# Kernel optimization log

Hardware: AMD Instinct MI355X
Metric: run time of the kernel (lower is better)

Reference implementation:

```python
import jax, jax.numpy as jnp
import numpy as np
import math

B, T, D, H = 2, 2048, 1024, 16
HD = D // H
FF = 4 * D
EPS = 1e-5


def rmsnorm(x, w):
    norm = jax.lax.rsqrt(jnp.mean(x * x, axis=-1, keepdims=True) + EPS)
    return x * norm * w


def setup_inputs() -> dict:
    key = jax.random.key(0)
    ks = jax.random.split(key, 10)
    s = 0.02
    x = jax.random.normal(ks[0], (B, T, D), dtype=jnp.float32)
    causal_mask = jnp.tril(jnp.ones((1, T, T), dtype=jnp.int32))
    # weights stored (in, out) so y = x @ W (equivalent to torch Linear with W.T)
    Wq = jax.random.normal(ks[1], (D, D), dtype=jnp.float32) * s
    Wk = jax.random.normal(ks[2], (D, D), dtype=jnp.float32) * s
    Wv = jax.random.normal(ks[3], (D, D), dtype=jnp.float32) * s
    Wo = jax.random.normal(ks[4], (D, D), dtype=jnp.float32) * s
    bo = jnp.zeros((D,), dtype=jnp.float32)
    W1 = jax.random.normal(ks[5], (D, FF), dtype=jnp.float32) * s
    b1 = jnp.zeros((FF,), dtype=jnp.float32)
    W2 = jax.random.normal(ks[6], (FF, D), dtype=jnp.float32) * s
    b2 = jnp.zeros((D,), dtype=jnp.float32)
    g_attn = jnp.ones((D,), dtype=jnp.float32)
    g_ff = jnp.ones((D,), dtype=jnp.float32)
    return dict(x=x, causal_mask=causal_mask, Wq=Wq, Wk=Wk, Wv=Wv, Wo=Wo, bo=bo,
                W1=W1, b1=b1, W2=W2, b2=b2, g_attn=g_attn, g_ff=g_ff)


def reference(x, causal_mask, Wq, Wk, Wv, Wo, bo, W1, b1, W2, b2, g_attn, g_ff):
    b, t, d = x.shape
    xa = rmsnorm(x, g_attn)
    # project and split heads: (b, h, t, hd)
    q = (xa @ Wq).reshape(b, t, H, HD).transpose(0, 2, 1, 3)
    k = (xa @ Wk).reshape(b, t, H, HD).transpose(0, 2, 1, 3)
    v = (xa @ Wv).reshape(b, t, H, HD).transpose(0, 2, 1, 3)
    scores = jnp.einsum('bhqd,bhkd->bhqk', q, k) / math.sqrt(HD)
    mask = causal_mask[:, None, :t, :t]  # (1,1,t,t)
    scores = jnp.where(mask == 0, jnp.float32(-1e9), scores)
    probs = jax.nn.softmax(scores, axis=-1)
    attn = jnp.einsum('bhqk,bhkd->bhqd', probs, v)
    attn = attn.transpose(0, 2, 1, 3).reshape(b, t, d)
    x = x + attn @ Wo + bo
    xf = rmsnorm(x, g_ff)
    h = jax.nn.silu(xf @ W1 + b1)
    x = x + h @ W2 + b2
    return x
```

## Files before the change

### kernel.cpp

```cpp
#include <hip/hip_runtime.h>
#include <hip/hip_bf16.h>
#include <cstdint>
#include <cstddef>

#define Bn 2
#define Tn 2048
#define Dn 1024
#define Hn 16
#define HDn 64
#define FFn 4096
#define Mrows (Bn*Tn)

typedef __bf16 bf16x8 __attribute__((ext_vector_type(8)));
typedef float  f32x4  __attribute__((ext_vector_type(4)));

__device__ __forceinline__ unsigned short f2bf(float f) {
  unsigned int u = __float_as_uint(f);
  unsigned int r = (u + 0x7FFFu + ((u >> 16) & 1u)) >> 16;
  return (unsigned short)r;
}

__device__ __forceinline__ void gload_lds16(const unsigned short* g, unsigned short* l) {
  __builtin_amdgcn_global_load_lds(
      (const __attribute__((address_space(1))) unsigned int*)g,
      (__attribute__((address_space(3))) unsigned int*)l, 16, 0, 0);
}

__device__ __forceinline__ f32x4 mfma16(bf16x8 a, bf16x8 b, f32x4 c) {
  return __builtin_amdgcn_mfma_f32_16x16x32_bf16(a, b, c, 0, 0, 0);
}

__global__ void cast_transpose(const float* __restrict__ in, unsigned short* __restrict__ out,
                               int R, int C) {
  __shared__ float tile[32][33];
  int c0 = blockIdx.x * 32, r0 = blockIdx.y * 32;
  int x = threadIdx.x, y = threadIdx.y;
  #pragma unroll
  for (int i = 0; i < 32; i += 8)
    tile[y + i][x] = in[(size_t)(r0 + y + i) * C + c0 + x];
  __syncthreads();
  #pragma unroll
  for (int i = 0; i < 32; i += 8)
    out[(size_t)(c0 + y + i) * R + r0 + x] = f2bf(tile[x][y + i]);
}

__global__ __launch_bounds__(256) void rmsnorm_cast(const float* __restrict__ x,
                                                    const float* __restrict__ g,
                                                    unsigned short* __restrict__ out) {
  __shared__ float ssum[4];
  int row = blockIdx.x;
  int tid = threadIdx.x;
  const float4* xr = (const float4*)(x + (size_t)row * Dn);
  float4 v = xr[tid];
  float ss = v.x * v.x + v.y * v.y + v.z * v.z + v.w * v.w;
  #pragma unroll
  for (int m = 32; m; m >>= 1) ss += __shfl_xor(ss, m);
  if ((tid & 63) == 0) ssum[tid >> 6] = ss;
  __syncthreads();
  float tot = ssum[0] + ssum[1] + ssum[2] + ssum[3];
  float nrm = rsqrtf(tot * (1.0f / Dn) + 1e-5f);
  float4 gv = ((const float4*)g)[tid];
  ushort4 o;
  o.x = f2bf(v.x * nrm * gv.x);
  o.y = f2bf(v.y * nrm * gv.y);
  o.z = f2bf(v.z * nrm * gv.z);
  o.w = f2bf(v.w * nrm * gv.w);
  ((ushort4*)out)[(size_t)row * (Dn / 4) + tid] = o;
}

#define BM 128
#define BN 128
#define BK 64
template <int EPI>
__global__ __launch_bounds__(256, 2) void gemm_bt(
    const unsigned short* __restrict__ A, const unsigned short* __restrict__ Bt,
    unsigned short* __restrict__ outB, unsigned short* __restrict__ outB2,
    unsigned short* __restrict__ outB3, float* __restrict__ outF,
    const float* __restrict__ bias, const float* __restrict__ resid,
    int Mdim, int Ndim, int Kdim) {
  __shared__ __align__(16) unsigned short As[BM * BK];
  __shared__ __align__(16) unsigned short Bs[BN * BK];
  const int tid = threadIdx.x;
  const int lane = tid & 63, w = tid >> 6;
  const int wr = w >> 1, wc = w & 1;
  const int lr = lane & 15, lg = lane >> 4;
  const int m0 = blockIdx.y * BM, n0 = blockIdx.x * BN;

  f32x4 acc[4][4] = {};
  const int kiters = Kdim / BK;
  for (int kt = 0; kt < kiters; ++kt) {
    const int k0 = kt * BK;
    #pragma unroll
    for (int i = 0; i < 4; ++i) {
      int c = tid + i * 256;
      int row = c >> 3, sl = c & 7, g = sl ^ (row & 7);
      gload_lds16(A + (size_t)(m0 + row) * Kdim + k0 + g * 8, &As[c * 8]);
    }
    #pragma unroll
    for (int i = 0; i < 4; ++i) {
      int c = tid + i * 256;
      int row = c >> 3, sl = c & 7, g = sl ^ (row & 7);
      gload_lds16(Bt + (size_t)(n0 + row) * Kdim + k0 + g * 8, &Bs[c * 8]);
    }
    asm volatile("s_waitcnt vmcnt(0)");
    __syncthreads();
    #pragma unroll
    for (int kk = 0; kk < 2; ++kk) {
      bf16x8 af[4], bfr[4];
      #pragma unroll
      for (int mi = 0; mi < 4; ++mi) {
        int row = wr * 64 + mi * 16 + lr;
        int sl = (kk * 4 + lg) ^ (row & 7);
        af[mi] = *(const bf16x8*)&As[row * BK + sl * 8];
      }
      #pragma unroll
      for (int ni = 0; ni < 4; ++ni) {
        int row = wc * 64 + ni * 16 + lr;
        int sl = (kk * 4 + lg) ^ (row & 7);
        bfr[ni] = *(const bf16x8*)&Bs[row * BK + sl * 8];
      }
      #pragma unroll
      for (int mi = 0; mi < 4; ++mi)
        #pragma unroll
        for (int ni = 0; ni < 4; ++ni)
          acc[mi][ni] = mfma16(af[mi], bfr[ni], acc[mi][ni]);
    }
    __syncthreads();
  }
  #pragma unroll
  for (int mi = 0; mi < 4; ++mi) {
    #pragma unroll
    for (int ni = 0; ni < 4; ++ni) {
      #pragma unroll
      for (int rg = 0; rg < 4; ++rg) {
        int r = m0 + wr * 64 + mi * 16 + lg * 4 + rg;
        int c = n0 + wc * 64 + ni * 16 + lr;
        float v = acc[mi][ni][rg];
        if (EPI == 0) {
          outB[(size_t)r * Ndim + c] = f2bf(v);
        } else if (EPI == 1) {
          int b = r >> 11, t = r & (Tn - 1);
          int hh = c >> 6, hd = c & 63;
          outB[(((size_t)((b * Hn + hh) * HDn + hd)) << 11) + t] = f2bf(v);
        } else if (EPI == 2) {
          outF[(size_t)r * Ndim + c] = v + bias[c] + resid[(size_t)r * Ndim + c];
        } else if (EPI == 3) {
          float vb = v + bias[c];
          float s = vb / (1.0f + __expf(-vb));
          outB[(size_t)r * Ndim + c] = f2bf(s);
        } else {
          if (n0 < Dn) {
            outB[(size_t)r * Dn + c] = f2bf(v);
          } else if (n0 < 2 * Dn) {
            outB2[(size_t)r * Dn + (c - Dn)] = f2bf(v);
          } else {
            int b = r >> 11, t = r & (Tn - 1);
            int cc = c - 2 * Dn;
            int hh = cc >> 6, hd = cc & 63;
            outB3[(((size_t)((b * Hn + hh) * HDn + hd)) << 11) + t] = f2bf(v);
          }
        }
      }
    }
  }
}

__global__ __launch_bounds__(256, 4) void attn_fwd(
    const unsigned short* __restrict__ Q, const unsigned short* __restrict__ Kb,
    const unsigned short* __restrict__ Vt, unsigned short* __restrict__ O) {
  __shared__ __align__(16) unsigned short Ks[2][64 * 64];
  __shared__ __align__(16) unsigned short Vs[2][64 * 64];
  __shared__ __align__(16) unsigned short Ps[4][16 * 64];
  const int tid = threadIdx.x, lane = tid & 63, w = tid >> 6;
  const int lr = lane & 15, lg = lane >> 4;
  const int id = blockIdx.x;
  const int bh = id >> 5, b = bh >> 4, h = bh & 15;
  const int qx = ((id & 31) + ((id >> 8) << 3)) & 31;
  const int qb = qx * 64;
  const int qw = qb + w * 16;

  const size_t qrow = ((size_t)(b * Tn) + qw + lr) * Dn + h * HDn;
  bf16x8 qf0 = *(const bf16x8*)&Q[qrow + lg * 8];
  bf16x8 qf1 = *(const bf16x8*)&Q[qrow + 32 + lg * 8];

  f32x4 ao[4] = {};
  float mrow[4], lsum[4];
  #pragma unroll
  for (int rg = 0; rg < 4; ++rg) { mrow[rg] = -1e30f; lsum[rg] = 0.f; }

  const int nkt = qx + 1;
  const size_t kbase = (size_t)(b * Tn) * Dn + h * HDn;
  const size_t vbase = ((size_t)((b * Hn + h) * HDn)) << 11;

  auto stage = [&](int buf, int kt) {
    #pragma unroll
    for (int i = 0; i < 2; ++i) {
      int c = tid + i * 256;
      int row = c >> 3, sl = c & 7, g = sl ^ (row & 7);
      gload_lds16(Kb + kbase + (size_t)(kt * 64 + row) * Dn + g * 8, &Ks[buf][c * 8]);
    }
    #pragma unroll
    for (int i = 0; i < 2; ++i) {
      int c = tid + i * 256;
      int row = c >> 3, sl = c & 7, g = sl ^ (row & 7);
      gload_lds16(Vt + vbase + ((size_t)row << 11) + kt * 64 + g * 8, &Vs[buf][c * 8]);
    }
  };

  stage(0, 0);
  __syncthreads();

  const float cl2 = 0.125f * 1.44269504f;

  for (int kt = 0; kt < nkt; ++kt) {
    const int cur = kt & 1;
    if (kt + 1 < nkt) stage(cur ^ 1, kt + 1);

    float p[4][4];
    #pragma unroll
    for (int sub = 0; sub < 4; ++sub) {
      f32x4 s = {};
      int row = sub * 16 + lr;
      bf16x8 k0 = *(const bf16x8*)&Ks[cur][row * 64 + ((0 + lg) ^ (row & 7)) * 8];
      bf16x8 k1 = *(const bf16x8*)&Ks[cur][row * 64 + ((4 + lg) ^ (row & 7)) * 8];
      s = mfma16(qf0, k0, s);
      s = mfma16(qf1, k1, s);
      #pragma unroll
      for (int rg = 0; rg < 4; ++rg) {
        int qg = qw + lg * 4 + rg;
        int kg = kt * 64 + sub * 16 + lr;
        p[sub][rg] = (kg > qg) ? -1e30f : s[rg] * cl2;
      }
    }
    #pragma unroll
    for (int rg = 0; rg < 4; ++rg) {
      float mt = fmaxf(fmaxf(p[0][rg], p[1][rg]), fmaxf(p[2][rg], p[3][rg]));
      #pragma unroll
      for (int msk = 1; msk < 16; msk <<= 1) mt = fmaxf(mt, __shfl_xor(mt, msk));
      float mnew = fmaxf(mrow[rg], mt);
      float sc = exp2f(mrow[rg] - mnew);
      float rs = 0.f;
      #pragma unroll
      for (int sub = 0; sub < 4; ++sub) {
        p[sub][rg] = exp2f(p[sub][rg] - mnew);
        rs += p[sub][rg];
      }
      #pragma unroll
      for (int msk = 1; msk < 16; msk <<= 1) rs += __shfl_xor(rs, msk);
      lsum[rg] = lsum[rg] * sc + rs;
      mrow[rg] = mnew;
      #pragma unroll
      for (int n = 0; n < 4; ++n) ao[n][rg] *= sc;
    }
    #pragma unroll
    for (int sub = 0; sub < 4; ++sub)
      #pragma unroll
      for (int rg = 0; rg < 4; ++rg) {
        int row = lg * 4 + rg;
        int col = sub * 16 + lr;
        int sl = (col >> 3) ^ (row & 7);
        Ps[w][row * 64 + sl * 8 + (col & 7)] = f2bf(p[sub][rg]);
      }
    bf16x8 pf0 = *(const bf16x8*)&Ps[w][lr * 64 + ((0 + lg) ^ (lr & 7)) * 8];
    bf16x8 pf1 = *(const bf16x8*)&Ps[w][lr * 64 + ((4 + lg) ^ (lr & 7)) * 8];
    #pragma unroll
    for (int n = 0; n < 4; ++n) {
      int vrow = n * 16 + lr;
      bf16x8 v0 = *(const bf16x8*)&Vs[cur][vrow * 64 + ((0 + lg) ^ (vrow & 7)) * 8];
      bf16x8 v1 = *(const bf16x8*)&Vs[cur][vrow * 64 + ((4 + lg) ^ (vrow & 7)) * 8];
      ao[n] = mfma16(pf0, v0, ao[n]);
      ao[n] = mfma16(pf1, v1, ao[n]);
    }
    __syncthreads();
  }
  #pragma unroll
  for (int rg = 0; rg < 4; ++rg) {
    float inv = 1.0f / lsum[rg];
    int r = b * Tn + qw + lg * 4 + rg;
    #pragma unroll
    for (int n = 0; n < 4; ++n)
      O[(size_t)r * Dn + h * HDn + n * 16 + lr] = f2bf(ao[n][rg] * inv);
  }
}

extern "C" void kernel_launch(void* const* d_in, const int* in_sizes, int n_in,
                              void* d_out, int out_size, void* d_ws, size_t ws_size,
                              hipStream_t stream) {
  const float* x      = (const float*)d_in[0];
  const float* Wq     = (const float*)d_in[2];
  const float* Wk     = (const float*)d_in[3];
  const float* Wv     = (const float*)d_in[4];
  const float* Wo     = (const float*)d_in[5];
  const float* bo     = (const float*)d_in[6];
  const float* W1     = (const float*)d_in[7];
  const float* b1     = (const float*)d_in[8];
  const float* W2     = (const float*)d_in[9];
  const float* b2     = (const float*)d_in[10];
  const float* g_attn = (const float*)d_in[11];
  const float* g_ff   = (const float*)d_in[12];
  float* out = (float*)d_out;

  char* ws = (char*)d_ws;
  size_t off = 0;
  auto carve = [&](size_t bytes) {
    void* p = ws + off;
    off += (bytes + 255) & ~(size_t)255;
    return p;
  };
  const size_t MD2 = (size_t)Mrows * Dn * 2;
  unsigned short* xa    = (unsigned short*)carve(MD2);
  unsigned short* qb    = (unsigned short*)carve(MD2);
  unsigned short* kb    = (unsigned short*)carve(MD2);
  unsigned short* vt    = (unsigned short*)carve(MD2);
  float*          xmid  = (float*)carve((size_t)Mrows * Dn * 4);
  unsigned short* hbuf  = (unsigned short*)carve((size_t)Mrows * FFn * 2);
  unsigned short* Wqkvt = (unsigned short*)carve((size_t)3 * Dn * Dn * 2);
  unsigned short* Wot   = (unsigned short*)carve((size_t)Dn * Dn * 2);
  unsigned short* W1t   = (unsigned short*)carve((size_t)Dn * FFn * 2);
  unsigned short* W2t   = (unsigned short*)carve((size_t)Dn * FFn * 2);

  dim3 tb(32, 8);
  cast_transpose<<<dim3(Dn / 32, Dn / 32), tb, 0, stream>>>(Wq, Wqkvt, Dn, Dn);
  cast_transpose<<<dim3(Dn / 32, Dn / 32), tb, 0, stream>>>(Wk, Wqkvt + (size_t)Dn * Dn, Dn, Dn);
  cast_transpose<<<dim3(Dn / 32, Dn / 32), tb, 0, stream>>>(Wv, Wqkvt + (size_t)2 * Dn * Dn, Dn, Dn);
  cast_transpose<<<dim3(Dn / 32, Dn / 32), tb, 0, stream>>>(Wo, Wot, Dn, Dn);
  cast_transpose<<<dim3(FFn / 32, Dn / 32), tb, 0, stream>>>(W1, W1t, Dn, FFn);
  cast_transpose<<<dim3(Dn / 32, FFn / 32), tb, 0, stream>>>(W2, W2t, FFn, Dn);

  rmsnorm_cast<<<Mrows, 256, 0, stream>>>(x, g_attn, xa);

  gemm_bt<4><<<dim3(3 * Dn / BN, Mrows / BM), 256, 0, stream>>>(
      xa, Wqkvt, qb, kb, vt, nullptr, nullptr, nullptr, Mrows, 3 * Dn, Dn);

  attn_fwd<<<dim3(1024), 256, 0, stream>>>(qb, kb, vt, xa);

  gemm_bt<2><<<dim3(Dn / BN, Mrows / BM), 256, 0, stream>>>(
      xa, Wot, nullptr, nullptr, nullptr, xmid, bo, x, Mrows, Dn, Dn);

  rmsnorm_cast<<<Mrows, 256, 0, stream>>>(xmid, g_ff, qb);

  gemm_bt<3><<<dim3(FFn / BN, Mrows / BM), 256, 0, stream>>>(
      qb, W1t, hbuf, nullptr, nullptr, nullptr, b1, nullptr, Mrows, FFn, Dn);
  gemm_bt<2><<<dim3(Dn / BN, Mrows / BM), 256, 0, stream>>>(
      hbuf, W2t, nullptr, nullptr, nullptr, out, b2, xmid, Mrows, Dn, FFn);
}
```

Measured before the change: 433.2 us.

## Pair causal attention tiles per block and split-K the FFN down-projection

The attention kernel now runs 512 threads per block, with two 256-thread groups handling complementary query tiles (pid and 31-pid) so every block does roughly equal causal work. It also skips mask arithmetic on fully unmasked key tiles, computes softmax row sums with an MFMA against a ones vector, and raises wave priority around the PV MFMAs. The W2 GEMM is split along K into two partial fp32 outputs written into the dead xa/q/k/v workspace, then a combine kernel adds both partials, the bias and the residual. The split adds an extra fp32 write/read pass and a kernel launch in exchange for more parallel blocks. The paired groups must also step through shared barriers up to the longer group's tile count.

```diff
diff --git a/kernel.cpp b/kernel.cpp
--- a/kernel.cpp
+++ b/kernel.cpp
@@ -77,7 +77,7 @@
     unsigned short* __restrict__ outB, unsigned short* __restrict__ outB2,
     unsigned short* __restrict__ outB3, float* __restrict__ outF,
     const float* __restrict__ bias, const float* __restrict__ resid,
-    int Mdim, int Ndim, int Kdim) {
+    int Mdim, int Ndim, int Kdim, int Kstride) {
   __shared__ __align__(16) unsigned short As[BM * BK];
   __shared__ __align__(16) unsigned short Bs[BN * BK];
   const int tid = threadIdx.x;
@@ -85,6 +85,11 @@
   const int wr = w >> 1, wc = w & 1;
   const int lr = lane & 15, lg = lane >> 4;
   const int m0 = blockIdx.y * BM, n0 = blockIdx.x * BN;
+  if (EPI == 5) {
+    size_t koff = (size_t)blockIdx.z * Kdim;
+    A += koff; Bt += koff;
+    outF += (size_t)blockIdx.z * Mdim * Ndim;
+  }
 
   f32x4 acc[4][4] = {};
   const int kiters = Kdim / BK;
@@ -94,13 +99,13 @@
     for (int i = 0; i < 4; ++i) {
       int c = tid + i * 256;
       int row = c >> 3, sl = c & 7, g = sl ^ (row & 7);
-      gload_lds16(A + (size_t)(m0 + row) * Kdim + k0 + g * 8, &As[c * 8]);
+      gload_lds16(A + (size_t)(m0 + row) * Kstride + k0 + g * 8, &As[c * 8]);
     }
     #pragma unroll
     for (int i = 0; i < 4; ++i) {
       int c = tid + i * 256;
       int row = c >> 3, sl = c & 7, g = sl ^ (row & 7);
-      gload_lds16(Bt + (size_t)(n0 + row) * Kdim + k0 + g * 8, &Bs[c * 8]);
+      gload_lds16(Bt + (size_t)(n0 + row) * Kstride + k0 + g * 8, &Bs[c * 8]);
     }
     asm volatile("s_waitcnt vmcnt(0)");
     __syncthreads();
@@ -138,17 +143,13 @@
         float v = acc[mi][ni][rg];
         if (EPI == 0) {
           outB[(size_t)r * Ndim + c] = f2bf(v);
-        } else if (EPI == 1) {
-          int b = r >> 11, t = r & (Tn - 1);
-          int hh = c >> 6, hd = c & 63;
-          outB[(((size_t)((b * Hn + hh) * HDn + hd)) << 11) + t] = f2bf(v);
         } else if (EPI == 2) {
           outF[(size_t)r * Ndim + c] = v + bias[c] + resid[(size_t)r * Ndim + c];
         } else if (EPI == 3) {
           float vb = v + bias[c];
           float s = vb / (1.0f + __expf(-vb));
           outB[(size_t)r * Ndim + c] = f2bf(s);
-        } else {
+        } else if (EPI == 4) {
           if (n0 < Dn) {
             outB[(size_t)r * Dn + c] = f2bf(v);
           } else if (n0 < 2 * Dn) {
@@ -159,23 +160,49 @@
             int hh = cc >> 6, hd = cc & 63;
             outB3[(((size_t)((b * Hn + hh) * HDn + hd)) << 11) + t] = f2bf(v);
           }
+        } else {
+          outF[(size_t)r * Ndim + c] = v;
         }
       }
     }
   }
 }
 
-__global__ __launch_bounds__(256, 4) void attn_fwd(
+__global__ __launch_bounds__(256) void combine2(const float* __restrict__ p0,
+                                                const float* __restrict__ p1,
+                                                const float* __restrict__ resid,
+                                                const float* __restrict__ bias,
+                                                float* __restrict__ out) {
+  int i = blockIdx.x * 256 + threadIdx.x;
+  float4 a = ((const float4*)p0)[i];
+  float4 b = ((const float4*)p1)[i];
+  float4 r = ((const float4*)resid)[i];
+  float4 bb = ((const float4*)bias)[i & 255];
+  float4 o;
+  o.x = a.x + b.x + r.x + bb.x;
+  o.y = a.y + b.y + r.y + bb.y;
+  o.z = a.z + b.z + r.z + bb.z;
+  o.w = a.w + b.w + r.w + bb.w;
+  ((float4*)out)[i] = o;
+}
+
+__global__ __launch_bounds__(512, 4) void attn_fwd(
     const unsigned short* __restrict__ Q, const unsigned short* __restrict__ Kb,
     const unsigned short* __restrict__ Vt, unsigned short* __restrict__ O) {
-  __shared__ __align__(16) unsigned short Ks[2][64 * 64];
-  __shared__ __align__(16) unsigned short Vs[2][64 * 64];
-  __shared__ __align__(16) unsigned short Ps[4][16 * 64];
-  const int tid = threadIdx.x, lane = tid & 63, w = tid >> 6;
+  __shared__ __align__(16) unsigned short Ks[2][2][64 * 64];
+  __shared__ __align__(16) unsigned short Vs[2][2][64 * 64];
+  __shared__ __align__(16) unsigned short Ps[2][4][16 * 64];
+  const int tid = threadIdx.x;
+  const int grp = tid >> 8;
+  const int t = tid & 255;
+  const int lane = tid & 63, w = (tid >> 6) & 3;
   const int lr = lane & 15, lg = lane >> 4;
   const int id = blockIdx.x;
-  const int bh = id >> 5, b = bh >> 4, h = bh & 15;
-  const int qx = ((id & 31) + ((id >> 8) << 3)) & 31;
+  const int bh = id >> 4, b = bh >> 4, h = bh & 15;
+  const int pid = id & 15;
+  const int qx = grp ? (31 - pid) : pid;
+  const int nkt = qx + 1;
+  const int nktmax = 32 - pid;
   const int qb = qx * 64;
   const int qw = qb + w * 16;
 
@@ -183,93 +210,106 @@
   bf16x8 qf0 = *(const bf16x8*)&Q[qrow + lg * 8];
   bf16x8 qf1 = *(const bf16x8*)&Q[qrow + 32 + lg * 8];
 
+  bf16x8 ones;
+  #pragma unroll
+  for (int j = 0; j < 8; ++j) ones[j] = (__bf16)1.0f;
+
   f32x4 ao[4] = {};
-  float mrow[4], lsum[4];
+  float mrow[4], lsum[4], sc[4];
   #pragma unroll
   for (int rg = 0; rg < 4; ++rg) { mrow[rg] = -1e30f; lsum[rg] = 0.f; }
 
-  const int nkt = qx + 1;
   const size_t kbase = (size_t)(b * Tn) * Dn + h * HDn;
   const size_t vbase = ((size_t)((b * Hn + h) * HDn)) << 11;
 
   auto stage = [&](int buf, int kt) {
     #pragma unroll
     for (int i = 0; i < 2; ++i) {
-      int c = tid + i * 256;
+      int c = t + i * 256;
       int row = c >> 3, sl = c & 7, g = sl ^ (row & 7);
-      gload_lds16(Kb + kbase + (size_t)(kt * 64 + row) * Dn + g * 8, &Ks[buf][c * 8]);
+      gload_lds16(Kb + kbase + (size_t)(kt * 64 + row) * Dn + g * 8, &Ks[grp][buf][c * 8]);
     }
     #pragma unroll
     for (int i = 0; i < 2; ++i) {
-      int c = tid + i * 256;
+      int c = t + i * 256;
       int row = c >> 3, sl = c & 7, g = sl ^ (row & 7);
-      gload_lds16(Vt + vbase + ((size_t)row << 11) + kt * 64 + g * 8, &Vs[buf][c * 8]);
+      gload_lds16(Vt + vbase + ((size_t)row << 11) + kt * 64 + g * 8, &Vs[grp][buf][c * 8]);
     }
   };
 
   stage(0, 0);
+  asm volatile("s_waitcnt vmcnt(0)");
   __syncthreads();
 
   const float cl2 = 0.125f * 1.44269504f;
 
-  for (int kt = 0; kt < nkt; ++kt) {
-    const int cur = kt & 1;
-    if (kt + 1 < nkt) stage(cur ^ 1, kt + 1);
-
-    float p[4][4];
-    #pragma unroll
-    for (int sub = 0; sub < 4; ++sub) {
-      f32x4 s = {};
-      int row = sub * 16 + lr;
-      bf16x8 k0 = *(const bf16x8*)&Ks[cur][row * 64 + ((0 + lg) ^ (row & 7)) * 8];
-      bf16x8 k1 = *(const bf16x8*)&Ks[cur][row * 64 + ((4 + lg) ^ (row & 7)) * 8];
-      s = mfma16(qf0, k0, s);
-      s = mfma16(qf1, k1, s);
+  for (int kt = 0; kt < nktmax; ++kt) {
+    const bool act = kt < nkt;
+    if (act) {
+      const int cur = kt & 1;
+      if (kt + 1 < nkt) stage(cur ^ 1, kt + 1);
+
+      float p[4][4];
+      const bool need_mask = (kt * 64 + 63) > qw;
+      #pragma unroll
+      for (int sub = 0; sub < 4; ++sub) {
+        f32x4 s = {};
+        int row = sub * 16 + lr;
+        bf16x8 k0 = *(const bf16x8*)&Ks[grp][cur][row * 64 + ((0 + lg) ^ (row & 7)) * 8];
+        bf16x8 k1 = *(const bf16x8*)&Ks[grp][cur][row * 64 + ((4 + lg) ^ (row & 7)) * 8];
+        s = mfma16(qf0, k0, s);
+        s = mfma16(qf1, k1, s);
+        if (need_mask) {
+          #pragma unroll
+          for (int rg = 0; rg < 4; ++rg) {
+            int qg = qw + lg * 4 + rg;
+            int kg = kt * 64 + sub * 16 + lr;
+            p[sub][rg] = (kg > qg) ? -1e30f : s[rg] * cl2;
+          }
+        } else {
+          #pragma unroll
+          for (int rg = 0; rg < 4; ++rg) p[sub][rg] = s[rg] * cl2;
+        }
+      }
       #pragma unroll
       for (int rg = 0; rg < 4; ++rg) {
-        int qg = qw + lg * 4 + rg;
-        int kg = kt * 64 + sub * 16 + lr;
-        p[sub][rg] = (kg > qg) ? -1e30f : s[rg] * cl2;
-      }
-    }
-    #pragma unroll
-    for (int rg = 0; rg < 4; ++rg) {
-      float mt = fmaxf(fmaxf(p[0][rg], p[1][rg]), fmaxf(p[2][rg], p[3][rg]));
-      #pragma unroll
-      for (int msk = 1; msk < 16; msk <<= 1) mt = fmaxf(mt, __shfl_xor(mt, msk));
-      float mnew = fmaxf(mrow[rg], mt);
-      float sc = exp2f(mrow[rg] - mnew);
-      float rs = 0.f;
-      #pragma unroll
-      for (int sub = 0; sub < 4; ++sub) {
-        p[sub][rg] = exp2f(p[sub][rg] - mnew);
-        rs += p[sub][rg];
-      }
-      #pragma unroll
-      for (int msk = 1; msk < 16; msk <<= 1) rs += __shfl_xor(rs, msk);
-      lsum[rg] = lsum[rg] * sc + rs;
-      mrow[rg] = mnew;
-      #pragma unroll
-      for (int n = 0; n < 4; ++n) ao[n][rg] *= sc;
-    }
-    #pragma unroll
-    for (int sub = 0; sub < 4; ++sub)
-      #pragma unroll
-      for (int rg = 0; rg < 4; ++rg) {
-        int row = lg * 4 + rg;
-        int col = sub * 16 + lr;
-        int sl = (col >> 3) ^ (row & 7);
-        Ps[w][row * 64 + sl * 8 + (col & 7)] = f2bf(p[sub][rg]);
-      }
-    bf16x8 pf0 = *(const bf16x8*)&Ps[w][lr * 64 + ((0 + lg) ^ (lr & 7)) * 8];
-    bf16x8 pf1 = *(const bf16x8*)&Ps[w][lr * 64 + ((4 + lg) ^ (lr & 7)) * 8];
-    #pragma unroll
-    for (int n = 0; n < 4; ++n) {
-      int vrow = n * 16 + lr;
-      bf16x8 v0 = *(const bf16x8*)&Vs[cur][vrow * 64 + ((0 + lg) ^ (vrow & 7)) * 8];
-      bf16x8 v1 = *(const bf16x8*)&Vs[cur][vrow * 64 + ((4 + lg) ^ (vrow & 7)) * 8];
-      ao[n] = mfma16(pf0, v0, ao[n]);
-      ao[n] = mfma16(pf1, v1, ao[n]);
+        float mt = fmaxf(fmaxf(p[0][rg], p[1][rg]), fmaxf(p[2][rg], p[3][rg]));
+        #pragma unroll
+        for (int msk = 1; msk < 16; msk <<= 1) mt = fmaxf(mt, __shfl_xor(mt, msk));
+        float mnew = fmaxf(mrow[rg], mt);
+        sc[rg] = exp2f(mrow[rg] - mnew);
+        #pragma unroll
+        for (int sub = 0; sub < 4; ++sub) p[sub][rg] = exp2f(p[sub][rg] - mnew);
+        mrow[rg] = mnew;
+        #pragma unroll
+        for (int n = 0; n < 4; ++n) ao[n][rg] *= sc[rg];
+      }
+      #pragma unroll
+      for (int sub = 0; sub < 4; ++sub)
+        #pragma unroll
+        for (int rg = 0; rg < 4; ++rg) {
+          int row = lg * 4 + rg;
+          int col = sub * 16 + lr;
+          int sl = (col >> 3) ^ (row & 7);
+          Ps[grp][w][row * 64 + sl * 8 + (col & 7)] = f2bf(p[sub][rg]);
+        }
+      bf16x8 pf0 = *(const bf16x8*)&Ps[grp][w][lr * 64 + ((0 + lg) ^ (lr & 7)) * 8];
+      bf16x8 pf1 = *(const bf16x8*)&Ps[grp][w][lr * 64 + ((4 + lg) ^ (lr & 7)) * 8];
+      __builtin_amdgcn_s_setprio(1);
+      f32x4 sl4 = {};
+      sl4 = mfma16(pf0, ones, sl4);
+      sl4 = mfma16(pf1, ones, sl4);
+      #pragma unroll
+      for (int n = 0; n < 4; ++n) {
+        int vrow = n * 16 + lr;
+        bf16x8 v0 = *(const bf16x8*)&Vs[grp][cur][vrow * 64 + ((0 + lg) ^ (vrow & 7)) * 8];
+        bf16x8 v1 = *(const bf16x8*)&Vs[grp][cur][vrow * 64 + ((4 + lg) ^ (vrow & 7)) * 8];
+        ao[n] = mfma16(pf0, v0, ao[n]);
+        ao[n] = mfma16(pf1, v1, ao[n]);
+      }
+      __builtin_amdgcn_s_setprio(0);
+      #pragma unroll
+      for (int rg = 0; rg < 4; ++rg) lsum[rg] = lsum[rg] * sc[rg] + sl4[rg];
     }
     __syncthreads();
   }
@@ -318,6 +358,7 @@
   unsigned short* Wot   = (unsigned short*)carve((size_t)Dn * Dn * 2);
   unsigned short* W1t   = (unsigned short*)carve((size_t)Dn * FFn * 2);
   unsigned short* W2t   = (unsigned short*)carve((size_t)Dn * FFn * 2);
+  float* w2part = (float*)xa;
 
   dim3 tb(32, 8);
   cast_transpose<<<dim3(Dn / 32, Dn / 32), tb, 0, stream>>>(Wq, Wqkvt, Dn, Dn);
@@ -330,17 +371,21 @@
   rmsnorm_cast<<<Mrows, 256, 0, stream>>>(x, g_attn, xa);
 
   gemm_bt<4><<<dim3(3 * Dn / BN, Mrows / BM), 256, 0, stream>>>(
-      xa, Wqkvt, qb, kb, vt, nullptr, nullptr, nullptr, Mrows, 3 * Dn, Dn);
-
-  attn_fwd<<<dim3(1024), 256, 0, stream>>>(qb, kb, vt, xa);
+      xa, Wqkvt, qb, kb, vt, nullptr, nullptr, nullptr, Mrows, 3 * Dn, Dn, Dn);
+
+  attn_fwd<<<dim3(512), 512, 0, stream>>>(qb, kb, vt, xa);
 
   gemm_bt<2><<<dim3(Dn / BN, Mrows / BM), 256, 0, stream>>>(
-      xa, Wot, nullptr, nullptr, nullptr, xmid, bo, x, Mrows, Dn, Dn);
+      xa, Wot, nullptr, nullptr, nullptr, xmid, bo, x, Mrows, Dn, Dn, Dn);
 
   rmsnorm_cast<<<Mrows, 256, 0, stream>>>(xmid, g_ff, qb);
 
   gemm_bt<3><<<dim3(FFn / BN, Mrows / BM), 256, 0, stream>>>(
-      qb, W1t, hbuf, nullptr, nullptr, nullptr, b1, nullptr, Mrows, FFn, Dn);
-  gemm_bt<2><<<dim3(Dn / BN, Mrows / BM), 256, 0, stream>>>(
-      hbuf, W2t, nullptr, nullptr, nullptr, out, b2, xmid, Mrows, Dn, FFn);
-}
+      qb, W1t, hbuf, nullptr, nullptr, nullptr, b1, nullptr, Mrows, FFn, Dn, Dn);
+
+  gemm_bt<5><<<dim3(Dn / BN, Mrows / BM, 2), 256, 0, stream>>>(
+      hbuf, W2t, nullptr, nullptr, nullptr, w2part, nullptr, nullptr,
+      Mrows, Dn, FFn / 2, FFn);
+  combine2<<<dim3((Mrows * Dn / 4) / 256), 256, 0, stream>>>(
+      w2part, w2part + (size_t)Mrows * Dn, xmid, b2, out);
+}
```

Measured after the change: 397.7 us. 8.2% less time.
